# Optimization experiments

Hardware: AMD Instinct MI355X
Metric: run time of the kernel (lower is better)

## Reference

```python
import jax, jax.numpy as jnp
import numpy as np

IN_C, H, W = 64, 256, 256
K = 3
OUT_C = 128


def setup_inputs() -> dict:
    key = jax.random.key(0)
    k1, k2 = jax.random.split(key)
    x = jax.random.normal(k1, (IN_C, H, W), dtype=jnp.float32)
    limit = np.sqrt(6.0 / (IN_C * K * K + OUT_C)).astype(np.float32)
    kernels = jax.random.uniform(k2, (OUT_C, IN_C, K, K), minval=-limit, maxval=limit, dtype=jnp.float32)
    biases = jnp.zeros((OUT_C,), dtype=jnp.float32)
    return {"x": x, "kernels": kernels, "biases": biases}


def reference(x, kernels, biases):
    # Cross-correlation (patch * kernel, no flip), VALID padding, CHW single image.
    out = jax.lax.conv_general_dilated(
        x[None],                      # [1, C, H, W]
        kernels,                      # [O, I, K, K]
        window_strides=(1, 1),
        padding="VALID",
        dimension_numbers=("NCHW", "OIHW", "NCHW"),
    )[0]                              # [O, H-K+1, W-K+1]
    return out + biases[:, None, None]
```

## Files before the change

kernel.cpp:

```cpp
#include <hip/hip_runtime.h>
#include <stdint.h>

#define IN_C 64
#define HH 256
#define WW 256
#define HW (HH * WW)
#define OUT_C 128
#define OH 254
#define OW 254
#define OHW (OH * OW)

#define XR 6
#define XW 66
#define CPAD 72

typedef __attribute__((ext_vector_type(4))) float f32x4;
typedef __attribute__((ext_vector_type(8))) __bf16 bf16x8;

__device__ __forceinline__ unsigned short f2bf(float f) {
  union { float f; unsigned u; } v; v.f = f;
  unsigned r = v.u + 0x7FFFu + ((v.u >> 16) & 1u);
  return (unsigned short)(r >> 16);
}

__global__ void prep_w(const float* __restrict__ w, unsigned short* __restrict__ wt) {
  const int idx = blockIdx.x * 256 + threadIdx.x;
  if (idx >= 9 * 8192) return;
  const int j    = idx & 7;
  const int lane = (idx >> 3) & 63;
  const int mt   = (idx >> 9) & 7;
  const int ch   = (idx >> 12) & 1;
  const int tap  = idx >> 13;
  const int o = mt * 16 + (lane & 15);
  const int c = ch * 32 + (lane >> 4) * 8 + j;
  wt[idx] = f2bf(w[(o * IN_C + c) * 9 + tap]);
}

__global__ __launch_bounds__(512, 2) void conv_mfma(
    const float* __restrict__ x, const unsigned short* __restrict__ wt,
    const float* __restrict__ bias, float* __restrict__ out) {
  __shared__ __align__(16) unsigned short Xs[XR * XW * CPAD];

  const int tid  = threadIdx.x;
  const int wave = tid >> 6;
  const int lane = tid & 63;
  const int x0 = blockIdx.x * 64;
  const int y0 = blockIdx.y * 4;

  const int mhalf = wave & 1;
  const int row   = wave >> 1;
  const int nlane = lane & 15;
  const int quad  = lane >> 4;

  const bf16x8* __restrict__ Wp = ((const bf16x8*)wt) + lane + (mhalf * 4) * 64;
  bf16x8 afA[4], afB[4];
#pragma unroll
  for (int mt = 0; mt < 4; ++mt) afA[mt] = Wp[mt * 64];

  {
    const int cq = tid & 15;
    const int xh = (tid >> 4) & 15;
    const int r3 = (tid >> 8) * 3;
#pragma unroll
    for (int k = 0; k < 3; ++k) {
      const int r = r3 + k;
      const int yr = (y0 + r > 255) ? 255 : (y0 + r);
      const float* bx = x + yr * WW + x0 + xh * 4;
      f32x4 vv[4];
#pragma unroll
      for (int cc = 0; cc < 4; ++cc)
        vv[cc] = *(const f32x4*)(bx + (cq * 4 + cc) * HW);
#pragma unroll
      for (int xxi = 0; xxi < 4; ++xxi) {
        unsigned u0 = (unsigned)f2bf(vv[0][xxi]) | ((unsigned)f2bf(vv[1][xxi]) << 16);
        unsigned u1 = (unsigned)f2bf(vv[2][xxi]) | ((unsigned)f2bf(vv[3][xxi]) << 16);
        *(uint2*)&Xs[(r * XW + xh * 4 + xxi) * CPAD + cq * 4] = make_uint2(u0, u1);
      }
    }
    for (int k = tid; k < 768; k += 512) {
      const int c = k & 63;
      const int q = k >> 6;
      const int xxt = 64 + (q & 1);
      const int r = q >> 1;
      const int yr = (y0 + r > 255) ? 255 : (y0 + r);
      int xg = x0 + xxt;
      if (xg > WW - 1) xg = WW - 1;
      Xs[(r * XW + xxt) * CPAD + c] = f2bf(x[c * HW + yr * WW + xg]);
    }
  }

  f32x4 acc[4][4];
#pragma unroll
  for (int mt = 0; mt < 4; ++mt) {
    const f32x4 bv = *(const f32x4*)(bias + (mhalf * 4 + mt) * 16 + quad * 4);
#pragma unroll
    for (int nt = 0; nt < 4; ++nt) acc[mt][nt] = bv;
  }

  __syncthreads();

#pragma unroll 1
  for (int pair = 0; pair < 9; ++pair) {
    const int ky = pair / 3;
    const int kx = pair - ky * 3;
    const int r = row + ky;
    const unsigned short* xrow = &Xs[(r * XW + kx) * CPAD + quad * 8];

#pragma unroll
    for (int mt = 0; mt < 4; ++mt) afB[mt] = Wp[((2 * pair + 1) * 8 + mt) * 64];

    {
      bf16x8 bfr[4];
#pragma unroll
      for (int nt = 0; nt < 4; ++nt)
        bfr[nt] = *(const bf16x8*)&xrow[(nt * 16 + nlane) * CPAD];
#pragma unroll
      for (int mt = 0; mt < 4; ++mt)
#pragma unroll
        for (int nt = 0; nt < 4; ++nt)
          acc[mt][nt] = __builtin_amdgcn_mfma_f32_16x16x32_bf16(afA[mt], bfr[nt], acc[mt][nt], 0, 0, 0);
    }

    if (pair < 8) {
#pragma unroll
      for (int mt = 0; mt < 4; ++mt) afA[mt] = Wp[((2 * pair + 2) * 8 + mt) * 64];
    }

    {
      bf16x8 bfr[4];
#pragma unroll
      for (int nt = 0; nt < 4; ++nt)
        bfr[nt] = *(const bf16x8*)&xrow[(nt * 16 + nlane) * CPAD + 32];
#pragma unroll
      for (int mt = 0; mt < 4; ++mt)
#pragma unroll
        for (int nt = 0; nt < 4; ++nt)
          acc[mt][nt] = __builtin_amdgcn_mfma_f32_16x16x32_bf16(afB[mt], bfr[nt], acc[mt][nt], 0, 0, 0);
    }
  }

  const int y = y0 + row;
  if (y < OH) {
#pragma unroll
    for (int mt = 0; mt < 4; ++mt) {
      const int obase = (mhalf * 4 + mt) * 16 + quad * 4;
#pragma unroll
      for (int nt = 0; nt < 4; ++nt) {
        const int xc = x0 + nt * 16 + nlane;
        if (xc < OW) {
          float* dst = out + obase * OHW + y * OW + xc;
#pragma unroll
          for (int reg = 0; reg < 4; ++reg)
            dst[reg * OHW] = acc[mt][nt][reg];
        }
      }
    }
  }
}

extern "C" void kernel_launch(void* const* d_in, const int* in_sizes, int n_in,
                              void* d_out, int out_size, void* d_ws, size_t ws_size,
                              hipStream_t stream) {
  const float* x = (const float*)d_in[0];
  const float* w = (const float*)d_in[1];
  const float* b = (const float*)d_in[2];
  float* out = (float*)d_out;
  unsigned short* wt = (unsigned short*)d_ws;

  prep_w<<<dim3(288), dim3(256), 0, stream>>>(w, wt);
  conv_mfma<<<dim3(4, 64), dim3(512), 0, stream>>>(x, wt, b, out);
}
```

Measured before the change: 88.52 us.

## Split input staging to overlap bottom-row loads with first-row MFMAs

The input tile load is split: rows 0-3 are staged before the barrier, while the global loads for rows 4-5 are issued early and written to LDS only after the first barrier. The first six MFMA chunks (ky=0, which need only rows 0-3) then run before a second barrier. The weight prefetch becomes a 3-deep register ring and the 18-chunk loop is fully unrolled. The aim is to hide global load latency behind compute, at the cost of one extra barrier and more live registers, which could hurt occupancy at 2 blocks per CU.

```diff
diff --git a/kernel.cpp b/kernel.cpp
--- a/kernel.cpp
+++ b/kernel.cpp
@@ -53,40 +53,58 @@
   const int quad  = lane >> 4;
 
   const bf16x8* __restrict__ Wp = ((const bf16x8*)wt) + lane + (mhalf * 4) * 64;
-  bf16x8 afA[4], afB[4];
-#pragma unroll
-  for (int mt = 0; mt < 4; ++mt) afA[mt] = Wp[mt * 64];
-
+  bf16x8 af[3][4];
+#pragma unroll
+  for (int mt = 0; mt < 4; ++mt) af[0][mt] = Wp[(0 * 8 + mt) * 64];
+#pragma unroll
+  for (int mt = 0; mt < 4; ++mt) af[1][mt] = Wp[(1 * 8 + mt) * 64];
+
+  const int cq = tid & 15;
+  const int xh = (tid >> 4) & 15;
+  const int z  = tid >> 8;
+
+#pragma unroll
+  for (int k = 0; k < 2; ++k) {
+    const int r = z * 2 + k;
+    const int yr = (y0 + r > 255) ? 255 : (y0 + r);
+    const float* bx = x + yr * WW + x0 + xh * 4;
+    f32x4 vv[4];
+#pragma unroll
+    for (int cc = 0; cc < 4; ++cc) vv[cc] = *(const f32x4*)(bx + (cq * 4 + cc) * HW);
+#pragma unroll
+    for (int xxi = 0; xxi < 4; ++xxi) {
+      unsigned u0 = (unsigned)f2bf(vv[0][xxi]) | ((unsigned)f2bf(vv[1][xxi]) << 16);
+      unsigned u1 = (unsigned)f2bf(vv[2][xxi]) | ((unsigned)f2bf(vv[3][xxi]) << 16);
+      *(uint2*)&Xs[(r * XW + xh * 4 + xxi) * CPAD + cq * 4] = make_uint2(u0, u1);
+    }
+  }
   {
-    const int cq = tid & 15;
-    const int xh = (tid >> 4) & 15;
-    const int r3 = (tid >> 8) * 3;
-#pragma unroll
-    for (int k = 0; k < 3; ++k) {
-      const int r = r3 + k;
-      const int yr = (y0 + r > 255) ? 255 : (y0 + r);
-      const float* bx = x + yr * WW + x0 + xh * 4;
-      f32x4 vv[4];
-#pragma unroll
-      for (int cc = 0; cc < 4; ++cc)
-        vv[cc] = *(const f32x4*)(bx + (cq * 4 + cc) * HW);
-#pragma unroll
-      for (int xxi = 0; xxi < 4; ++xxi) {
-        unsigned u0 = (unsigned)f2bf(vv[0][xxi]) | ((unsigned)f2bf(vv[1][xxi]) << 16);
-        unsigned u1 = (unsigned)f2bf(vv[2][xxi]) | ((unsigned)f2bf(vv[3][xxi]) << 16);
-        *(uint2*)&Xs[(r * XW + xh * 4 + xxi) * CPAD + cq * 4] = make_uint2(u0, u1);
-      }
-    }
-    for (int k = tid; k < 768; k += 512) {
-      const int c = k & 63;
-      const int q = k >> 6;
-      const int xxt = 64 + (q & 1);
-      const int r = q >> 1;
-      const int yr = (y0 + r > 255) ? 255 : (y0 + r);
-      int xg = x0 + xxt;
-      if (xg > WW - 1) xg = WW - 1;
-      Xs[(r * XW + xxt) * CPAD + c] = f2bf(x[c * HW + yr * WW + xg]);
-    }
+    const int c = tid & 63;
+    const int q = tid >> 6;
+    const int xxt = 64 + (q & 1);
+    const int r = q >> 1;
+    const int yr = (y0 + r > 255) ? 255 : (y0 + r);
+    int xg = x0 + xxt;
+    if (xg > WW - 1) xg = WW - 1;
+    Xs[(r * XW + xxt) * CPAD + c] = f2bf(x[c * HW + yr * WW + xg]);
+  }
+
+  f32x4 vv2[4];
+  float hv2;
+  {
+    const int r = 4 + z;
+    const int yr = (y0 + r > 255) ? 255 : (y0 + r);
+    const float* bx = x + yr * WW + x0 + xh * 4;
+#pragma unroll
+    for (int cc = 0; cc < 4; ++cc) vv2[cc] = *(const f32x4*)(bx + (cq * 4 + cc) * HW);
+    const int c = tid & 63;
+    const int q = (tid >> 6) & 3;
+    const int xxt = 64 + (q & 1);
+    const int rh = 4 + (q >> 1);
+    const int yrh = (y0 + rh > 255) ? 255 : (y0 + rh);
+    int xg = x0 + xxt;
+    if (xg > WW - 1) xg = WW - 1;
+    hv2 = x[c * HW + yrh * WW + xg];
   }
 
   f32x4 acc[4][4];
@@ -99,45 +117,55 @@
 
   __syncthreads();
 
-#pragma unroll 1
-  for (int pair = 0; pair < 9; ++pair) {
-    const int ky = pair / 3;
-    const int kx = pair - ky * 3;
-    const int r = row + ky;
-    const unsigned short* xrow = &Xs[(r * XW + kx) * CPAD + quad * 8];
-
-#pragma unroll
-    for (int mt = 0; mt < 4; ++mt) afB[mt] = Wp[((2 * pair + 1) * 8 + mt) * 64];
-
-    {
-      bf16x8 bfr[4];
-#pragma unroll
-      for (int nt = 0; nt < 4; ++nt)
-        bfr[nt] = *(const bf16x8*)&xrow[(nt * 16 + nlane) * CPAD];
-#pragma unroll
-      for (int mt = 0; mt < 4; ++mt)
-#pragma unroll
-        for (int nt = 0; nt < 4; ++nt)
-          acc[mt][nt] = __builtin_amdgcn_mfma_f32_16x16x32_bf16(afA[mt], bfr[nt], acc[mt][nt], 0, 0, 0);
-    }
-
-    if (pair < 8) {
-#pragma unroll
-      for (int mt = 0; mt < 4; ++mt) afA[mt] = Wp[((2 * pair + 2) * 8 + mt) * 64];
-    }
-
-    {
-      bf16x8 bfr[4];
-#pragma unroll
-      for (int nt = 0; nt < 4; ++nt)
-        bfr[nt] = *(const bf16x8*)&xrow[(nt * 16 + nlane) * CPAD + 32];
-#pragma unroll
-      for (int mt = 0; mt < 4; ++mt)
-#pragma unroll
-        for (int nt = 0; nt < 4; ++nt)
-          acc[mt][nt] = __builtin_amdgcn_mfma_f32_16x16x32_bf16(afB[mt], bfr[nt], acc[mt][nt], 0, 0, 0);
-    }
-  }
+  {
+    const int r = 4 + z;
+#pragma unroll
+    for (int xxi = 0; xxi < 4; ++xxi) {
+      unsigned u0 = (unsigned)f2bf(vv2[0][xxi]) | ((unsigned)f2bf(vv2[1][xxi]) << 16);
+      unsigned u1 = (unsigned)f2bf(vv2[2][xxi]) | ((unsigned)f2bf(vv2[3][xxi]) << 16);
+      *(uint2*)&Xs[(r * XW + xh * 4 + xxi) * CPAD + cq * 4] = make_uint2(u0, u1);
+    }
+    if (tid < 256) {
+      const int c = tid & 63;
+      const int q = (tid >> 6) & 3;
+      const int xxt = 64 + (q & 1);
+      const int rh = 4 + (q >> 1);
+      Xs[(rh * XW + xxt) * CPAD + c] = f2bf(hv2);
+    }
+  }
+
+#define PF(c)                                                                  \
+  if ((c) < 18) {                                                              \
+    _Pragma("unroll")                                                          \
+    for (int mt = 0; mt < 4; ++mt) af[(c) % 3][mt] = Wp[((c) * 8 + mt) * 64];  \
+  }
+#define COMP(c)                                                                \
+  {                                                                            \
+    const int tap = (c) >> 1, ky = tap / 3, kx = tap - ky * 3;                 \
+    const unsigned short* xrow = &Xs[((row + ky) * XW + kx) * CPAD +           \
+                                     quad * 8 + ((c) & 1) * 32];               \
+    bf16x8 bfr[4];                                                             \
+    _Pragma("unroll")                                                          \
+    for (int nt = 0; nt < 4; ++nt)                                             \
+      bfr[nt] = *(const bf16x8*)&xrow[(nt * 16 + nlane) * CPAD];               \
+    _Pragma("unroll")                                                          \
+    for (int mt = 0; mt < 4; ++mt)                                             \
+      _Pragma("unroll")                                                        \
+      for (int nt = 0; nt < 4; ++nt)                                           \
+        acc[mt][nt] = __builtin_amdgcn_mfma_f32_16x16x32_bf16(                 \
+            af[(c) % 3][mt], bfr[nt], acc[mt][nt], 0, 0, 0);                   \
+  }
+
+#pragma unroll
+  for (int c = 0; c < 6; ++c) { PF(c + 2); COMP(c); }
+
+  __syncthreads();
+
+#pragma unroll
+  for (int c = 6; c < 18; ++c) { PF(c + 2); COMP(c); }
+
+#undef PF
+#undef COMP
 
   const int y = y0 + row;
   if (y < OH) {
```

Measured after the change: 98.31 us. 11.1% more time.
